# Kernel tuning notes

Hardware: AMD Instinct MI355X
Metric: run time of the kernel (lower is better)

Reference implementation:

```python
import jax, jax.numpy as jnp
import numpy as np

N_NODES = 50000
N_EDGES = 800000
IN_DIM = 256
HID = [256, 128]
NEG_SLOPE = 0.01  # F.leaky_relu default


def setup_inputs() -> dict:
    key = jax.random.key(0)
    ks = jax.random.split(key, 8)
    x = jax.random.normal(ks[0], (N_NODES, IN_DIM), dtype=jnp.float32)
    w1 = jax.random.normal(ks[1], (IN_DIM, HID[0]), dtype=jnp.float32) * (1.0 / np.sqrt(IN_DIM))
    b1 = jnp.zeros((HID[0],), dtype=jnp.float32)
    w2 = jax.random.normal(ks[2], (HID[0], HID[1]), dtype=jnp.float32) * (1.0 / np.sqrt(HID[0]))
    b2 = jnp.zeros((HID[1],), dtype=jnp.float32)
    src = jax.random.randint(ks[3], (N_EDGES,), 0, N_NODES, dtype=jnp.int32)
    dst = jax.random.randint(ks[4], (N_EDGES,), 0, N_NODES, dtype=jnp.int32)
    edge_weight = jax.random.uniform(ks[5], (N_EDGES,), dtype=jnp.float32)
    return {"x": x, "w1": w1, "b1": b1, "w2": w2, "b2": b2,
            "src": src, "dst": dst, "edge_weight": edge_weight}


def _gcn_layer(h, w, b, src, dst, ew, n_nodes):
    # GraphConvolution: support = h @ W ; out = spmm(adj, support) + b
    support = h @ w                              # [N, d_out]
    msg = support[src] * ew[:, None]             # [E, d_out] gather + scale
    agg = jax.ops.segment_sum(msg, dst, num_segments=n_nodes)  # [N, d_out]
    return agg + b


def reference(x, w1, b1, w2, b2, src, dst, edge_weight):
    # layer 1: GCN -> leaky_relu -> dropout(eval: identity)
    h = _gcn_layer(x, w1, b1, src, dst, edge_weight, N_NODES)
    h = jax.nn.leaky_relu(h, NEG_SLOPE)
    # layer 2
    h = _gcn_layer(h, w2, b2, src, dst, edge_weight, N_NODES)
    h = jax.nn.leaky_relu(h, NEG_SLOPE)
    return h
```

## Files before the change

kernel.cpp:

```cpp
#include <hip/hip_runtime.h>

#define NEG_SLOPE 0.01f

constexpr int N_NODES_C = 50000;
constexpr int N_EDGES_C = 800000;
constexpr int M_PAD = 50048;
constexpr int META_CAP = 950016;

typedef short bf16x8 __attribute__((ext_vector_type(8)));
typedef float f32x4 __attribute__((ext_vector_type(4)));

__device__ inline unsigned short f2bf(float f) {
  unsigned int u = __float_as_uint(f);
  u += 0x7FFF + ((u >> 16) & 1);
  return (unsigned short)(u >> 16);
}
__device__ inline float bf2f(unsigned int h16) {
  return __uint_as_float(h16 << 16);
}

constexpr int NB_CONVX = (M_PAD * 32) / 256;
constexpr int NB_W1 = (256 * 256) / 256;
constexpr int NB_W2 = (256 * 128) / 256;
constexpr int NB_HIST = ((N_EDGES_C / 4) + 255) / 256;
constexpr int NB_PRE = NB_CONVX + NB_W1 + NB_W2 + NB_HIST;

__global__ __launch_bounds__(256) void pre_kernel(
    const float* __restrict__ x, const float* __restrict__ w1,
    const float* __restrict__ w2, const int* __restrict__ dst,
    unsigned short* __restrict__ xb, unsigned short* __restrict__ w1T,
    unsigned short* __restrict__ w2T, int* __restrict__ counts) {
  const int bx = blockIdx.x;
  const int tid = threadIdx.x;
  if (bx < NB_CONVX) {
    int idx = bx * 256 + tid;
    int row = idx >> 5;
    int c8 = (idx & 31) << 3;
    uint4 v;
    if (row < N_NODES_C) {
      const float4* p = (const float4*)(x + (size_t)row * 256 + c8);
      float4 a = p[0], b = p[1];
      v.x = f2bf(a.x) | ((unsigned)f2bf(a.y) << 16);
      v.y = f2bf(a.z) | ((unsigned)f2bf(a.w) << 16);
      v.z = f2bf(b.x) | ((unsigned)f2bf(b.y) << 16);
      v.w = f2bf(b.z) | ((unsigned)f2bf(b.w) << 16);
    } else {
      v = make_uint4(0, 0, 0, 0);
    }
    *(uint4*)(xb + (size_t)row * 256 + c8) = v;
  } else if (bx < NB_CONVX + NB_W1) {
    int idx = (bx - NB_CONVX) * 256 + tid;
    int n = idx >> 8, k = idx & 255;
    w1T[idx] = f2bf(w1[(size_t)k * 256 + n]);
  } else if (bx < NB_CONVX + NB_W1 + NB_W2) {
    int idx = (bx - NB_CONVX - NB_W1) * 256 + tid;
    int n = idx >> 8, k = idx & 255;
    w2T[idx] = f2bf(w2[(size_t)k * 128 + n]);
  } else {
    int g = (bx - NB_CONVX - NB_W1 - NB_W2) * 256 + tid;
    int e = g * 4;
    if (e < N_EDGES_C) {
      int4 d4 = *(const int4*)(dst + e);
      atomicAdd(&counts[d4.x], 1);
      atomicAdd(&counts[d4.y], 1);
      atomicAdd(&counts[d4.z], 1);
      atomicAdd(&counts[d4.w], 1);
    }
  }
}

constexpr int NB_NODE = (N_NODES_C + 255) / 256;
constexpr int NB_SCAT = (M_PAD + 255) / 256;

__global__ __launch_bounds__(256) void hist_kernel(const int* __restrict__ counts,
                                                   int* __restrict__ hist2,
                                                   int* __restrict__ ehist) {
  __shared__ int lh[64], le[64];
  const int t = threadIdx.x;
  if (t < 64) { lh[t] = 0; le[t] = 0; }
  __syncthreads();
  const int i = blockIdx.x * 256 + t;
  if (i < N_NODES_C) {
    int d = counts[i];
    int bin = d < 63 ? d : 63;
    atomicAdd(&lh[bin], 1);
    atomicAdd(&le[bin], (d + 3) & ~3);
  }
  __syncthreads();
  if (t < 64) {
    if (lh[t]) atomicAdd(&hist2[t], lh[t]);
    if (le[t]) atomicAdd(&ehist[t], le[t]);
  }
}

__global__ __launch_bounds__(256) void scatter_kernel(
    const int* __restrict__ counts, const int* __restrict__ hist2,
    const int* __restrict__ ehist, int* __restrict__ gclaim_n,
    int* __restrict__ gclaim_e, int* __restrict__ perm,
    int* __restrict__ nstart, int* __restrict__ ndeg,
    int* __restrict__ cursor, unsigned* __restrict__ s_meta) {
  __shared__ int nbase[64], ebase[64], lh[64], le[64], gn[64], ge[64];
  const int t = threadIdx.x;
  if (t < 64) {
    int hv = hist2[t], ev = ehist[t];
    int xs = hv, xe = ev;
#pragma unroll
    for (int off = 1; off < 64; off <<= 1) {
      int a = __shfl_up(xs, off);
      int b = __shfl_up(xe, off);
      if (t >= off) { xs += a; xe += b; }
    }
    nbase[t] = xs - hv;
    ebase[t] = xe - ev;
    lh[t] = 0;
    le[t] = 0;
  }
  __syncthreads();
  const int idx = blockIdx.x * 256 + t;
  int d = -1, bin = 0, lrank = 0, erank = 0;
  if (idx < N_NODES_C) {
    d = counts[idx];
    bin = d < 63 ? d : 63;
    lrank = atomicAdd(&lh[bin], 1);
    erank = atomicAdd(&le[bin], (d + 3) & ~3);
  } else if (idx < M_PAD) {
    perm[idx] = idx;
    nstart[idx] = 0;
    ndeg[idx] = 0;
  }
  __syncthreads();
  if (t < 64) {
    gn[t] = lh[t] ? nbase[t] + atomicAdd(&gclaim_n[t], lh[t]) : 0;
    ge[t] = le[t] ? ebase[t] + atomicAdd(&gclaim_e[t], le[t]) : 0;
  }
  __syncthreads();
  if (d >= 0) {
    const int grank = gn[bin] + lrank;
    const int estart = ge[bin] + erank;
    perm[grank] = idx;
    nstart[grank] = estart;
    ndeg[grank] = d;
    cursor[idx] = estart;
    const int d4 = (d + 3) & ~3;
    for (int j = d; j < d4; ++j) s_meta[estart + j] = 0;
  }
}


#define GLOAD_LDS16(g, l)                                              \
  __builtin_amdgcn_global_load_lds(                                    \
      (__attribute__((address_space(1))) void*)(g),                    \
      (__attribute__((address_space(3))) void*)(l), 16, 0, 0)

__device__ __forceinline__ void gemm_tile(
    const unsigned short* __restrict__ A,
    const unsigned short* __restrict__ BT,
    unsigned short* __restrict__ C,
    int N, int row0, int col0, short* Asm, short* Bsm) {
  constexpr int K = 256;
  const int tid = threadIdx.x;
  const int lane = tid & 63, wave = tid >> 6;
  const int wm = wave & 1, wn = wave >> 1;

  const int ch0 = wave * 2, ch1 = wave * 2 + 1;
  const int o0 = ch0 * 512 + lane * 8;
  const int o1 = ch1 * 512 + lane * 8;
  const int r0 = o0 >> 5, c0 = o0 & 31;
  const int r1 = o1 >> 5, c1 = o1 & 31;

  f32x4 acc[4][4] = {};

  for (int k0 = 0; k0 < K; k0 += 32) {
    GLOAD_LDS16(A + (size_t)(row0 + r0) * K + k0 + c0, &Asm[ch0 * 512]);
    GLOAD_LDS16(A + (size_t)(row0 + r1) * K + k0 + c1, &Asm[ch1 * 512]);
    GLOAD_LDS16(BT + (size_t)(col0 + r0) * K + k0 + c0, &Bsm[ch0 * 512]);
    GLOAD_LDS16(BT + (size_t)(col0 + r1) * K + k0 + c1, &Bsm[ch1 * 512]);
    __builtin_amdgcn_s_waitcnt(0);
    __syncthreads();

    bf16x8 af[4], bf[4];
#pragma unroll
    for (int mt = 0; mt < 4; ++mt)
      af[mt] = *(const bf16x8*)&Asm[(wm * 64 + mt * 16 + (lane & 15)) * 32 + (lane >> 4) * 8];
#pragma unroll
    for (int nt = 0; nt < 4; ++nt)
      bf[nt] = *(const bf16x8*)&Bsm[(wn * 64 + nt * 16 + (lane & 15)) * 32 + (lane >> 4) * 8];
#pragma unroll
    for (int mt = 0; mt < 4; ++mt)
#pragma unroll
      for (int nt = 0; nt < 4; ++nt)
        acc[mt][nt] = __builtin_amdgcn_mfma_f32_16x16x32_bf16(af[mt], bf[nt], acc[mt][nt], 0, 0, 0);
    __syncthreads();
  }

  const int cl = lane & 15, rq = (lane >> 4) * 4;
#pragma unroll
  for (int mt = 0; mt < 4; ++mt) {
    const int rbase = row0 + wm * 64 + mt * 16 + rq;
#pragma unroll
    for (int nt = 0; nt < 4; ++nt) {
      const int col = col0 + wn * 64 + nt * 16 + cl;
      const size_t sbase = ((size_t)(col >> 5) * M_PAD) * 32 + (col & 31);
#pragma unroll
      for (int i = 0; i < 4; ++i)
        C[sbase + (size_t)(rbase + i) * 32] = f2bf(acc[mt][nt][i]);
    }
  }
}

constexpr int NB_GEMM1 = 2 * (M_PAD / 128);
constexpr int NB_FILL = ((N_EDGES_C / 4) + 255) / 256;

__global__ __launch_bounds__(256) void fill_gemm1_kernel(
    const unsigned short* __restrict__ A, const unsigned short* __restrict__ BT,
    unsigned short* __restrict__ C, const int* __restrict__ src,
    const int* __restrict__ dst, const float* __restrict__ ew,
    int* __restrict__ cursor, unsigned* __restrict__ s_meta) {
  __shared__ short Asm[128 * 32];
  __shared__ short Bsm[128 * 32];
  const int b = blockIdx.x;
  if ((b & 1) == 0) {
    const int t = b >> 1;
    gemm_tile(A, BT, C, 256, (t >> 1) * 128, (t & 1) * 128, Asm, Bsm);
  } else {
    const int g = (b >> 1) * 256 + threadIdx.x;
    const int e = g * 4;
    if (e < N_EDGES_C) {
      int4 d4 = *(const int4*)(dst + e);
      int4 s4 = *(const int4*)(src + e);
      float4 w4 = *(const float4*)(ew + e);
      unsigned m0 = (unsigned)s4.x | ((unsigned)f2bf(w4.x) << 16);
      unsigned m1 = (unsigned)s4.y | ((unsigned)f2bf(w4.y) << 16);
      unsigned m2 = (unsigned)s4.z | ((unsigned)f2bf(w4.z) << 16);
      unsigned m3 = (unsigned)s4.w | ((unsigned)f2bf(w4.w) << 16);
      int p0 = atomicAdd(&cursor[d4.x], 1);
      int p1 = atomicAdd(&cursor[d4.y], 1);
      int p2 = atomicAdd(&cursor[d4.z], 1);
      int p3 = atomicAdd(&cursor[d4.w], 1);
      __builtin_nontemporal_store(m0, s_meta + p0);
      __builtin_nontemporal_store(m1, s_meta + p1);
      __builtin_nontemporal_store(m2, s_meta + p2);
      __builtin_nontemporal_store(m3, s_meta + p3);
    }
  }
}

__global__ __launch_bounds__(256) void gemm2_kernel(
    const unsigned short* __restrict__ A, const unsigned short* __restrict__ BT,
    unsigned short* __restrict__ C) {
  __shared__ short Asm[128 * 32];
  __shared__ short Bsm[128 * 32];
  gemm_tile(A, BT, C, 128, blockIdx.x * 128, 0, Asm, Bsm);
}


__device__ inline void fma8(float* acc, uint4 v, float wt) {
  acc[0] += bf2f(v.x & 0xffffu) * wt;
  acc[1] += bf2f(v.x >> 16) * wt;
  acc[2] += bf2f(v.y & 0xffffu) * wt;
  acc[3] += bf2f(v.y >> 16) * wt;
  acc[4] += bf2f(v.z & 0xffffu) * wt;
  acc[5] += bf2f(v.z >> 16) * wt;
  acc[6] += bf2f(v.w & 0xffffu) * wt;
  acc[7] += bf2f(v.w >> 16) * wt;
}

__device__ __forceinline__ void gfma4(float* acc, uint4 m,
                                      const unsigned short* __restrict__ tab,
                                      int dimg) {
  uint4 v0 = *(const uint4*)(tab + (m.x & 0xffffu) * 32 + dimg * 8);
  uint4 v1 = *(const uint4*)(tab + (m.y & 0xffffu) * 32 + dimg * 8);
  uint4 v2 = *(const uint4*)(tab + (m.z & 0xffffu) * 32 + dimg * 8);
  uint4 v3 = *(const uint4*)(tab + (m.w & 0xffffu) * 32 + dimg * 8);
  fma8(acc, v0, bf2f(m.x >> 16));
  fma8(acc, v1, bf2f(m.y >> 16));
  fma8(acc, v2, bf2f(m.z >> 16));
  fma8(acc, v3, bf2f(m.w >> 16));
}

template <int NSLICE, int OUT_D, bool OUT_BF16>
__global__ __launch_bounds__(64) void agg_lite_kernel(
    const unsigned short* __restrict__ supS,
    const unsigned* __restrict__ s_meta,
    const int* __restrict__ nstart, const int* __restrict__ ndeg,
    const int* __restrict__ perm, const float* __restrict__ bias,
    unsigned short* __restrict__ out_bf, float* __restrict__ out_f, int n_total) {
  const int bx = blockIdx.x;
  const int slice = bx & (NSLICE - 1);
  const int group = bx / NSLICE;
  const int lane = threadIdx.x;
  const int quad = lane >> 2;
  const int dimg = lane & 3;
  const int idx = group * 16 + quad;
  if (idx >= n_total) return;
  const int n = perm[idx];
  const bool valid = n < N_NODES_C;
  const unsigned short* tab = supS + (size_t)slice * M_PAD * 32;

  float acc[8] = {};
  const int s = nstart[idx];
  const int nq = (ndeg[idx] + 3) >> 2;
  const uint4* mp = (const uint4*)(s_meta + s);

  if (nq > 0) {
    uint4 m0 = mp[0];
    uint4 m1 = (nq > 1) ? mp[1] : make_uint4(0, 0, 0, 0);
    int q = 0;
    for (; q + 2 < nq; q += 2) {
      uint4 p0 = mp[q + 2];
      uint4 p1 = mp[q + 3];
      gfma4(acc, m0, tab, dimg);
      gfma4(acc, m1, tab, dimg);
      m0 = p0;
      m1 = p1;
    }
    gfma4(acc, m0, tab, dimg);
    if (q + 1 < nq) gfma4(acc, m1, tab, dimg);
  }

  const int dbase = slice * 32 + dimg * 8;
  if (OUT_BF16) {
    unsigned short o[8];
#pragma unroll
    for (int j = 0; j < 8; ++j) {
      if (valid) {
        float v = acc[j] + bias[dbase + j];
        v = v >= 0.f ? v : NEG_SLOPE * v;
        o[j] = f2bf(v);
      } else {
        o[j] = 0;
      }
    }
    uint4 pk;
    pk.x = o[0] | ((unsigned)o[1] << 16);
    pk.y = o[2] | ((unsigned)o[3] << 16);
    pk.z = o[4] | ((unsigned)o[5] << 16);
    pk.w = o[6] | ((unsigned)o[7] << 16);
    *(uint4*)(out_bf + (size_t)n * OUT_D + dbase) = pk;
  } else if (valid) {
    float r[8];
#pragma unroll
    for (int j = 0; j < 8; ++j) {
      float v = acc[j] + bias[dbase + j];
      r[j] = v >= 0.f ? v : NEG_SLOPE * v;
    }
    *(float4*)(out_f + (size_t)n * OUT_D + dbase) = make_float4(r[0], r[1], r[2], r[3]);
    *(float4*)(out_f + (size_t)n * OUT_D + dbase + 4) = make_float4(r[4], r[5], r[6], r[7]);
  }
}


extern "C" void kernel_launch(void* const* d_in, const int* in_sizes, int n_in,
                              void* d_out, int out_size, void* d_ws, size_t ws_size,
                              hipStream_t stream) {
  const float* x  = (const float*)d_in[0];
  const float* w1 = (const float*)d_in[1];
  const float* b1 = (const float*)d_in[2];
  const float* w2 = (const float*)d_in[3];
  const float* b2 = (const float*)d_in[4];
  const int*   src = (const int*)d_in[5];
  const int*   dst = (const int*)d_in[6];
  const float* ew  = (const float*)d_in[7];
  float* out = (float*)d_out;

  unsigned short* xb   = (unsigned short*)d_ws;
  unsigned short* a2b  = xb + (size_t)M_PAD * 256;
  unsigned short* sup1 = a2b + (size_t)M_PAD * 256;
  unsigned short* sup2 = sup1 + (size_t)M_PAD * 256;
  unsigned short* w1T  = sup2 + (size_t)M_PAD * 128;
  unsigned short* w2T  = w1T + 256 * 256;
  int* counts  = (int*)(w2T + 128 * 256);
  int* cursor  = counts + N_NODES_C;
  int* perm    = cursor + N_NODES_C;
  int* nstart  = perm + M_PAD;
  int* ndeg    = nstart + M_PAD;
  int* hist2   = ndeg + M_PAD;
  int* ehist   = hist2 + 64;
  int* gclaim_n= ehist + 64;
  int* gclaim_e= gclaim_n + 64;
  unsigned* s_meta = (unsigned*)(gclaim_e + 64);

  hipMemsetAsync(counts, 0, N_NODES_C * sizeof(int), stream);
  hipMemsetAsync(hist2, 0, 256 * sizeof(int), stream);
  pre_kernel<<<NB_PRE, 256, 0, stream>>>(x, w1, w2, dst, xb, w1T, w2T, counts);

  hist_kernel<<<NB_NODE, 256, 0, stream>>>(counts, hist2, ehist);
  scatter_kernel<<<NB_SCAT, 256, 0, stream>>>(counts, hist2, ehist, gclaim_n,
                                              gclaim_e, perm, nstart, ndeg,
                                              cursor, s_meta);

  fill_gemm1_kernel<<<NB_GEMM1 + NB_FILL, 256, 0, stream>>>(
      xb, w1T, sup1, src, dst, ew, cursor, s_meta);

  agg_lite_kernel<8, 256, true><<<(M_PAD / 16) * 8, 64, 0, stream>>>(
      sup1, s_meta, nstart, ndeg, perm, b1, a2b, nullptr, M_PAD);

  gemm2_kernel<<<M_PAD / 128, 256, 0, stream>>>(a2b, w2T, sup2);
  agg_lite_kernel<4, 128, false><<<(N_NODES_C / 16) * 4, 64, 0, stream>>>(
      sup2, s_meta, nstart, ndeg, perm, b2, nullptr, out, N_NODES_C);
}
```

Measured before the change: 287.6 us.

## Interleave histogram blocks, widen x conversion per thread, enlarge aggregation blocks

```diff
diff --git a/kernel.cpp b/kernel.cpp
--- a/kernel.cpp
+++ b/kernel.cpp
@@ -19,11 +19,13 @@
   return __uint_as_float(h16 << 16);
 }
 
-constexpr int NB_CONVX = (M_PAD * 32) / 256;
+constexpr int NB_CONVX = (M_PAD * 8) / 256;
 constexpr int NB_W1 = (256 * 256) / 256;
 constexpr int NB_W2 = (256 * 128) / 256;
 constexpr int NB_HIST = ((N_EDGES_C / 4) + 255) / 256;
-constexpr int NB_PRE = NB_CONVX + NB_W1 + NB_W2 + NB_HIST;
+constexpr int NB_NONH = NB_CONVX + NB_W1 + NB_W2;
+constexpr int NB_PRE = NB_NONH + NB_HIST;
+constexpr int NB_IL = 2 * NB_HIST;
 
 __global__ __launch_bounds__(256) void pre_kernel(
     const float* __restrict__ x, const float* __restrict__ w1,
@@ -32,33 +34,16 @@
     unsigned short* __restrict__ w2T, int* __restrict__ counts) {
   const int bx = blockIdx.x;
   const int tid = threadIdx.x;
-  if (bx < NB_CONVX) {
-    int idx = bx * 256 + tid;
-    int row = idx >> 5;
-    int c8 = (idx & 31) << 3;
-    uint4 v;
-    if (row < N_NODES_C) {
-      const float4* p = (const float4*)(x + (size_t)row * 256 + c8);
-      float4 a = p[0], b = p[1];
-      v.x = f2bf(a.x) | ((unsigned)f2bf(a.y) << 16);
-      v.y = f2bf(a.z) | ((unsigned)f2bf(a.w) << 16);
-      v.z = f2bf(b.x) | ((unsigned)f2bf(b.y) << 16);
-      v.w = f2bf(b.z) | ((unsigned)f2bf(b.w) << 16);
-    } else {
-      v = make_uint4(0, 0, 0, 0);
-    }
-    *(uint4*)(xb + (size_t)row * 256 + c8) = v;
-  } else if (bx < NB_CONVX + NB_W1) {
-    int idx = (bx - NB_CONVX) * 256 + tid;
-    int n = idx >> 8, k = idx & 255;
-    w1T[idx] = f2bf(w1[(size_t)k * 256 + n]);
-  } else if (bx < NB_CONVX + NB_W1 + NB_W2) {
-    int idx = (bx - NB_CONVX - NB_W1) * 256 + tid;
-    int n = idx >> 8, k = idx & 255;
-    w2T[idx] = f2bf(w2[(size_t)k * 128 + n]);
+  int l = 0, isHist = 0, h = 0;
+  if (bx < NB_IL) {
+    if (bx & 1) { isHist = 1; h = bx >> 1; }
+    else l = bx >> 1;
   } else {
-    int g = (bx - NB_CONVX - NB_W1 - NB_W2) * 256 + tid;
-    int e = g * 4;
+    l = bx - NB_HIST;
+  }
+
+  if (isHist) {
+    int e = (h * 256 + tid) * 4;
     if (e < N_EDGES_C) {
       int4 d4 = *(const int4*)(dst + e);
       atomicAdd(&counts[d4.x], 1);
@@ -66,6 +51,38 @@
       atomicAdd(&counts[d4.z], 1);
       atomicAdd(&counts[d4.w], 1);
     }
+  } else if (l < NB_CONVX) {
+    int idx = l * 256 + tid;
+    int row = idx >> 3;
+    int c32 = (idx & 7) * 32;
+    uint4 o[4];
+    if (row < N_NODES_C) {
+      const float4* p = (const float4*)(x + (size_t)row * 256 + c32);
+      float4 f[8];
+#pragma unroll
+      for (int i = 0; i < 8; ++i) f[i] = p[i];
+#pragma unroll
+      for (int i = 0; i < 4; ++i) {
+        o[i].x = f2bf(f[2 * i].x) | ((unsigned)f2bf(f[2 * i].y) << 16);
+        o[i].y = f2bf(f[2 * i].z) | ((unsigned)f2bf(f[2 * i].w) << 16);
+        o[i].z = f2bf(f[2 * i + 1].x) | ((unsigned)f2bf(f[2 * i + 1].y) << 16);
+        o[i].w = f2bf(f[2 * i + 1].z) | ((unsigned)f2bf(f[2 * i + 1].w) << 16);
+      }
+    } else {
+#pragma unroll
+      for (int i = 0; i < 4; ++i) o[i] = make_uint4(0, 0, 0, 0);
+    }
+#pragma unroll
+    for (int i = 0; i < 4; ++i)
+      *(uint4*)(xb + (size_t)row * 256 + c32 + i * 8) = o[i];
+  } else if (l < NB_CONVX + NB_W1) {
+    int idx = (l - NB_CONVX) * 256 + tid;
+    int n = idx >> 8, k = idx & 255;
+    w1T[idx] = f2bf(w1[(size_t)k * 256 + n]);
+  } else {
+    int idx = (l - NB_CONVX - NB_W1) * 256 + tid;
+    int n = idx >> 8, k = idx & 255;
+    w2T[idx] = f2bf(w2[(size_t)k * 128 + n]);
   }
 }
 
@@ -279,7 +296,7 @@
 }
 
 template <int NSLICE, int OUT_D, bool OUT_BF16>
-__global__ __launch_bounds__(64) void agg_lite_kernel(
+__global__ __launch_bounds__(256) void agg_lite_kernel(
     const unsigned short* __restrict__ supS,
     const unsigned* __restrict__ s_meta,
     const int* __restrict__ nstart, const int* __restrict__ ndeg,
@@ -288,10 +305,11 @@
   const int bx = blockIdx.x;
   const int slice = bx & (NSLICE - 1);
   const int group = bx / NSLICE;
-  const int lane = threadIdx.x;
-  const int quad = lane >> 2;
-  const int dimg = lane & 3;
-  const int idx = group * 16 + quad;
+  const int tid = threadIdx.x;
+  const int wv = tid >> 6;
+  const int quad = (tid & 63) >> 2;
+  const int dimg = tid & 3;
+  const int idx = group * 64 + wv * 16 + quad;
   if (idx >= n_total) return;
   const int n = perm[idx];
   const bool valid = n < N_NODES_C;
@@ -392,10 +410,10 @@
   fill_gemm1_kernel<<<NB_GEMM1 + NB_FILL, 256, 0, stream>>>(
       xb, w1T, sup1, src, dst, ew, cursor, s_meta);
 
-  agg_lite_kernel<8, 256, true><<<(M_PAD / 16) * 8, 64, 0, stream>>>(
+  agg_lite_kernel<8, 256, true><<<(M_PAD / 64) * 8, 256, 0, stream>>>(
       sup1, s_meta, nstart, ndeg, perm, b1, a2b, nullptr, M_PAD);
 
   gemm2_kernel<<<M_PAD / 128, 256, 0, stream>>>(a2b, w2T, sup2);
-  agg_lite_kernel<4, 128, false><<<(N_NODES_C / 16) * 4, 64, 0, stream>>>(
+  agg_lite_kernel<4, 128, false><<<((N_NODES_C + 63) / 64) * 4, 256, 0, stream>>>(
       sup2, s_meta, nstart, ndeg, perm, b2, nullptr, out, N_NODES_C);
 }
```

After: 283.3 us. No clear change (-1.5%).
